# Kernel optimization log

Hardware: AMD Instinct MI355X
Metric: run time of the kernel (lower is better)

Reference implementation:

```python
import jax, jax.numpy as jnp
import numpy as np
from jax import lax

KS = 3
R = KS // 2
DILATIONS = (1, 3, 5)


def _fused_ddpm(x, kernels):
    """x: [N,C,H,W]; kernels: [N,3,C,KS*KS,H,W] -> [N,4C,H,W].
    Branch 0 is identity (x); branches 1..3 are per-pixel depthwise conv
    with dilations 1,3,5, zero padding, kernel taken at the output pixel."""
    N, C, H, W = x.shape
    outs = [x]
    for bi, d in enumerate(DILATIONS):
        pad = R * d
        xp = jnp.pad(x, ((0, 0), (0, 0), (pad, pad), (pad, pad)))
        acc = jnp.zeros_like(x)
        for ki in range(KS):
            for kj in range(KS):
                # shifted window: offset (ki-R)*d, (kj-R)*d relative to center
                patch = xp[:, :, ki * d:ki * d + H, kj * d:kj * d + W]
                acc = acc + patch * kernels[:, bi, :, ki * KS + kj]
        outs.append(acc)
    return jnp.concatenate(outs, axis=1)  # [N,4C,H,W]


def setup_inputs() -> dict:
    key = jax.random.key(0)
    k1, k2, k3, k4, k5, k6 = jax.random.split(key, 6)
    N, C, H, W = 4, 64, 128, 128
    x = jax.random.normal(k1, (N, C, H, W), dtype=jnp.float32)
    y = jax.random.normal(k2, (N, C, H, W), dtype=jnp.float32)
    # generator: Conv2d(C, 3*C*KS^2, 1) -> weight [3*C*9, C], bias [3*C*9]
    gen_w = jax.random.normal(k3, (3 * C * KS * KS, C), dtype=jnp.float32) * (1.0 / np.sqrt(C))
    gen_b = jax.random.normal(k4, (3 * C * KS * KS,), dtype=jnp.float32) * 0.01
    # fuse: Conv2d(4C, C, 3, 1, 1) -> weight [C, 4C, 3, 3], bias [C]
    fuse_w = jax.random.normal(k5, (C, 4 * C, 3, 3), dtype=jnp.float32) * (1.0 / np.sqrt(4 * C * 9))
    fuse_b = jax.random.normal(k6, (C,), dtype=jnp.float32) * 0.01
    return {"x": x, "y": y, "gen_w": gen_w, "gen_b": gen_b,
            "fuse_w": fuse_w, "fuse_b": fuse_b}


def reference(x, y, gen_w, gen_b, fuse_w, fuse_b):
    N, C, H, W = x.shape
    # 1x1 conv generator: per-pixel kernels
    k = jnp.einsum('oc,nchw->nohw', gen_w, y) + gen_b[None, :, None, None]
    kernels = k.reshape(N, 3, C, KS * KS, H, W)
    cat_out = _fused_ddpm(x, kernels)  # [N,4C,H,W]
    out = lax.conv_general_dilated(
        cat_out, fuse_w, window_strides=(1, 1), padding=((1, 1), (1, 1)),
        dimension_numbers=('NCHW', 'OIHW', 'NCHW'))
    return out + fuse_b[None, :, None, None]
```

## Files before the change

kernel.cpp:

```cpp
#include <hip/hip_runtime.h>


using f32x4 = __attribute__((ext_vector_type(4))) float;
using u32x4 = __attribute__((ext_vector_type(4))) unsigned;
using s16x8 = __attribute__((ext_vector_type(8))) short;

#define XP_PS 20160

#define OFF_WPK 0u
#define OFF_FW3 55296u
#define OFF_GBP 129024u
#define OFF_XP  131072u
#define OFF_CATP 4325376u

__device__ __forceinline__ unsigned short f2bf(float f) {
    unsigned u = __builtin_bit_cast(unsigned, f);
    u = (u + 0x7fffu + ((u >> 16) & 1u)) >> 16;
    return (unsigned short)u;
}
__device__ __forceinline__ float bflo(unsigned p) {
    return __builtin_bit_cast(float, p << 16);
}
__device__ __forceinline__ float bfhi(unsigned p) {
    return __builtin_bit_cast(float, p & 0xffff0000u);
}

__global__ void k_prep(const float* __restrict__ gen_w,
                       const float* __restrict__ gen_b,
                       const float* __restrict__ fuse_w,
                       const float* __restrict__ x,
                       float* __restrict__ ws) {
    int b = blockIdx.x;
    int t = threadIdx.x;
    if (b < 54) {
        int idx = b * 256 + t;
        if (idx >= 13824) return;
        unsigned short* wpk = (unsigned short*)(ws + OFF_WPK);
        int lane = idx & 63;
        int r = idx >> 6;
        int ks = r & 1; r >>= 1;
        int tile = r % 12, tap = r / 12;
        int comb = tile * 16 + (lane & 15);
        int cc0  = ks * 32 + (lane >> 4) * 8;
        const float* src = gen_w + (size_t)(comb * 9 + tap) * 64 + cc0;
        unsigned short v[8];
#pragma unroll
        for (int j = 0; j < 8; ++j) v[j] = f2bf(src[j]);
        *(s16x8*)(wpk + (size_t)idx * 8) = *(const s16x8*)v;
    } else if (b < 61) {
        int idx = (b - 54) * 256 + t;
        if (idx >= 1728) return;
        int row = idx & 15;
        int r = idx >> 4;
        int tile = r % 12, tap = r / 12;
        ws[OFF_GBP + idx] = gen_b[(tile * 16 + row) * 9 + tap];
    } else if (b < 133) {
        int idx = (b - 61) * 256 + t;
        if (idx >= 18432) return;
        unsigned short* fw3 = (unsigned short*)(ws + OFF_FW3);
        int lane = idx & 63;
        int f = idx >> 6;
        int rt = f & 3; f >>= 2;
        int ks = f & 1; f >>= 1;
        int chunk = f & 3;
        int g = f >> 2;
        int oc = rt * 16 + (lane & 15);
        int ic = chunk * 64 + ks * 32 + (lane >> 4) * 8;
        const float* src = fuse_w + (size_t)oc * 2304 + (size_t)ic * 9 + g;
        unsigned short v[8];
#pragma unroll
        for (int j = 0; j < 8; ++j) v[j] = f2bf(src[j * 9]);
        *(s16x8*)(fw3 + (size_t)idx * 8) = *(const s16x8*)v;
    } else {
        int idx = (b - 133) * 256 + t;
        unsigned* xp = (unsigned*)(ws + OFF_XP);
        int plane = idx / 5040;
        int rem   = idx % 5040;
        int row   = rem / 36;
        int c4    = rem % 36;
        u32x4 v = (u32x4){0u, 0u, 0u, 0u};
        if (row >= 5 && row < 133 && c4 >= 2 && c4 < 34) {
            const float* sx = x + (size_t)(2 * plane) * 16384 +
                              (row - 5) * 128 + (c4 * 4 - 8);
            f32x4 v0 = *(const f32x4*)sx;
            f32x4 v1 = *(const f32x4*)(sx + 16384);
#pragma unroll
            for (int j = 0; j < 4; ++j)
                v[j] = (unsigned)f2bf(v0[j]) | ((unsigned)f2bf(v1[j]) << 16);
        }
        *(u32x4*)(xp + (size_t)plane * XP_PS + row * 144 + c4 * 4) = v;
    }
}

__device__ __forceinline__ void decode_wu(int id, int& h, int& w0, int& n) {
    int wu = (id & 7) * 128 + (id >> 3);
    h = wu & 127;
    int sn = wu >> 7;
    w0 = (sn & 1) << 6;
    n = sn >> 1;
}

__global__ __launch_bounds__(256, 4) void k_gen_mfma(
    const unsigned* __restrict__ xp, const float* __restrict__ y,
    const unsigned short* __restrict__ wpk, const float* __restrict__ gbp,
    unsigned* __restrict__ catp)
{
    __shared__ __align__(16) unsigned Yt[2048];

    int h, w0, n;
    decode_wu(blockIdx.x, h, w0, n);
    const int t = threadIdx.x;
    const int lane = t & 63;
    const int wv = t >> 6;
    const int q = lane >> 4, col = lane & 15;

    {
        const float* yb = y + ((size_t)n * 64) * 16384 + h * 128 + w0 + lane;
#pragma unroll
        for (int p = 0; p < 8; ++p) {
            int cp = wv * 8 + p;
            float a = yb[(size_t)(2 * cp) * 16384];
            float b = yb[(size_t)(2 * cp + 1) * 16384];
            unsigned v = (unsigned)f2bf(a) | ((unsigned)f2bf(b) << 16);
            Yt[(unsigned)(lane * 32 + cp) ^ (((unsigned)(lane & 7)) << 2)] = v;
        }
    }
    __syncthreads();

    s16x8 bfr[4][2];
#pragma unroll
    for (int ctp = 0; ctp < 4; ++ctp)
#pragma unroll
        for (int ks = 0; ks < 2; ++ks) {
            int px = ctp * 16 + col;
            unsigned word = ((unsigned)(px * 32 + ks * 16 + q * 4)) ^
                            (((unsigned)(px & 7)) << 2);
            bfr[ctp][ks] = *(const s16x8*)(Yt + word);
        }

    const int tile0 = wv * 3;
    const unsigned* xn = xp + (size_t)n * 32 * XP_PS;

    float acc[3][4][4];
#pragma unroll
    for (int rt = 0; rt < 3; ++rt)
#pragma unroll
        for (int ctp = 0; ctp < 4; ++ctp)
#pragma unroll
            for (int r = 0; r < 4; ++r) acc[rt][ctp][r] = 0.f;

#pragma unroll 1
    for (int tap = 0; tap < 9; ++tap) {
        const int ti = tap / 3, tj = tap % 3;
        const unsigned short* wp = wpk + ((size_t)(tap * 12 + tile0) * 2 * 64 + lane) * 8;
#pragma unroll
        for (int rt = 0; rt < 3; ++rt) {
            const int tile = tile0 + rt;
            const int bi = tile >> 2;
            const int d  = 2 * bi + 1;
            const int hh = h + (ti - 1) * d;
            const int cb = (tile & 3) * 16 + q * 4;

            f32x4 cinit = *(const f32x4*)(gbp + (size_t)(tap * 12 + tile) * 16 + q * 4);
            s16x8 a0 = *(const s16x8*)(wp + (size_t)(rt * 2 + 0) * 512);
            s16x8 a1 = *(const s16x8*)(wp + (size_t)(rt * 2 + 1) * 512);
#pragma unroll
            for (int ctp = 0; ctp < 4; ++ctp) {
                f32x4 kf = __builtin_amdgcn_mfma_f32_16x16x32_bf16(a0, bfr[ctp][0], cinit, 0, 0, 0);
                kf = __builtin_amdgcn_mfma_f32_16x16x32_bf16(a1, bfr[ctp][1], kf, 0, 0, 0);
                const int ww = w0 + ctp * 16 + col + (tj - 1) * d;
                const unsigned* xr = xn + (size_t)(cb >> 1) * XP_PS +
                                     (hh + 5) * 144 + (ww + 8);
                unsigned p0 = xr[0];
                unsigned p1 = xr[XP_PS];
                acc[rt][ctp][0] = fmaf(kf[0], bflo(p0), acc[rt][ctp][0]);
                acc[rt][ctp][1] = fmaf(kf[1], bfhi(p0), acc[rt][ctp][1]);
                acc[rt][ctp][2] = fmaf(kf[2], bflo(p1), acc[rt][ctp][2]);
                acc[rt][ctp][3] = fmaf(kf[3], bfhi(p1), acc[rt][ctp][3]);
            }
        }
    }

    unsigned* cb0 = catp + (size_t)n * 96 * 16384 + h * 128;
#pragma unroll
    for (int rt = 0; rt < 3; ++rt) {
        const int combr = (tile0 + rt) * 16 + q * 4;
#pragma unroll
        for (int ctp = 0; ctp < 4; ++ctp) {
            const int px = w0 + ctp * 16 + col;
            unsigned v0 = (unsigned)f2bf(acc[rt][ctp][0]) |
                          ((unsigned)f2bf(acc[rt][ctp][1]) << 16);
            unsigned v1 = (unsigned)f2bf(acc[rt][ctp][2]) |
                          ((unsigned)f2bf(acc[rt][ctp][3]) << 16);
            cb0[(size_t)((combr >> 1) + 0) * 16384 + px] = v0;
            cb0[(size_t)((combr >> 1) + 1) * 16384 + px] = v1;
        }
    }
}

__global__ __launch_bounds__(256) void k_fuse_mfma(
    const unsigned* __restrict__ xp, const unsigned* __restrict__ catp,
    const unsigned short* __restrict__ fw3, const float* __restrict__ fuse_b,
    float* __restrict__ out)
{
    __shared__ __align__(16) unsigned Xt[4 * 32 * 68];

    const int id = blockIdx.x;
    const int xcd = id & 7;
    const int unit = id >> 3;
    const int h0 = unit << 1;
    const int n  = xcd >> 1;
    const int w0 = (xcd & 1) << 6;

    const int t = threadIdx.x;
    const int lane = t & 63;
    const int ctp = t >> 6;
    const int col = lane & 15, q = lane >> 4;

    int s_r[8], s_cp[8], s_li[8];
#pragma unroll
    for (int it = 0; it < 8; ++it) {
        int e = it * 256 + t;
        s_r[it]  = e >> 9;
        s_cp[it] = (e >> 4) & 31;
        s_li[it] = e & 15;
    }
    const int hr = t >> 6, hcp = (t >> 1) & 31, hside = t & 1;
    const int hpx = hside ? (w0 + 64) : (w0 - 1);
    const bool hok = ((unsigned)hpx < 128u);

    const int bcol = ctp * 16 + col;
    const int m_kw[3] = { (bcol == 0) ? 64 : bcol - 1,
                          bcol,
                          (bcol == 63) ? 65 : bcol + 1 };

    f32x4 acc[2][4];
#pragma unroll
    for (int row = 0; row < 2; ++row)
#pragma unroll
        for (int rt = 0; rt < 4; ++rt) acc[row][rt] = (f32x4){0.f, 0.f, 0.f, 0.f};

    const unsigned* csrc[4] = {
        nullptr,
        catp + (size_t)n * 96 * 16384,
        catp + ((size_t)n * 96 + 32) * 16384,
        catp + ((size_t)n * 96 + 64) * 16384 };

    u32x4 pf[8];
    unsigned pfh;
    {
        const unsigned* src0 = xp + (size_t)n * 32 * XP_PS;
#pragma unroll
        for (int it = 0; it < 8; ++it)
            pf[it] = *(const u32x4*)(src0 + (size_t)s_cp[it] * XP_PS +
                                     (h0 + 4 + s_r[it]) * 144 + 8 + w0 + s_li[it] * 4);
        pfh = src0[(size_t)hcp * XP_PS + (h0 + 4 + hr) * 144 + 8 + hpx];
    }

#pragma unroll 1
    for (int chunk = 0; chunk < 4; ++chunk) {
        s16x8 afc[4];
        {
            const unsigned short* ap =
                fw3 + ((size_t)(((chunk * 2 + 0) * 4) * 64 + lane)) * 8;
#pragma unroll
            for (int rt = 0; rt < 4; ++rt)
                afc[rt] = *(const s16x8*)(ap + (size_t)rt * 512);
        }

#pragma unroll
        for (int it = 0; it < 8; ++it)
            *(u32x4*)(Xt + (s_r[it] * 32 + s_cp[it]) * 68 + s_li[it] * 4) = pf[it];
        Xt[(hr * 32 + hcp) * 68 + 64 + hside] = pfh;

        if (chunk < 3) {
            const unsigned* src = csrc[chunk + 1];
#pragma unroll
            for (int it = 0; it < 8; ++it) {
                int hh = h0 - 1 + s_r[it];
                u32x4 v = (u32x4){0u, 0u, 0u, 0u};
                if ((unsigned)hh < 128u)
                    v = *(const u32x4*)(src + (size_t)s_cp[it] * 16384 + hh * 128 + w0 + s_li[it] * 4);
                pf[it] = v;
            }
            int hh = h0 - 1 + hr;
            unsigned v = 0u;
            if (hok && (unsigned)hh < 128u)
                v = src[(size_t)hcp * 16384 + hh * 128 + hpx];
            pfh = v;
        }
        __syncthreads();

#pragma unroll
        for (int i = 0; i < 18; ++i) {
            const int g = i >> 1, ks = i & 1;
            const int kh = g / 3, kw = g % 3;

            s16x8 afn[4];
            if (i < 17) {
                const int g2 = (i + 1) >> 1, ks2 = (i + 1) & 1;
                const unsigned short* ap = fw3 +
                    ((size_t)((((g2 * 4 + chunk) * 2 + ks2) * 4) * 64 + lane)) * 8;
#pragma unroll
                for (int rt = 0; rt < 4; ++rt)
                    afn[rt] = *(const s16x8*)(ap + (size_t)rt * 512);
            }

            const int cpb = ks * 16 + q * 4;
            const int mm = m_kw[kw];
            s16x8 bf[2];
#pragma unroll
            for (int row = 0; row < 2; ++row) {
                const unsigned* bp = Xt + ((row + kh) * 32 + cpb) * 68 + mm;
                unsigned bb[4] = {bp[0], bp[68], bp[136], bp[204]};
                bf[row] = *(const s16x8*)bb;
            }
#pragma unroll
            for (int rt = 0; rt < 4; ++rt)
#pragma unroll
                for (int row = 0; row < 2; ++row)
                    acc[row][rt] = __builtin_amdgcn_mfma_f32_16x16x32_bf16(
                        afc[rt], bf[row], acc[row][rt], 0, 0, 0);

            if (i < 17) {
#pragma unroll
                for (int rt = 0; rt < 4; ++rt) afc[rt] = afn[rt];
            }
        }
        __syncthreads();
    }

    const int px = w0 + ctp * 16 + col;
#pragma unroll
    for (int rt = 0; rt < 4; ++rt) {
        f32x4 fb = *(const f32x4*)(fuse_b + rt * 16 + q * 4);
#pragma unroll
        for (int row = 0; row < 2; ++row)
#pragma unroll
            for (int r = 0; r < 4; ++r) {
                int oc = rt * 16 + q * 4 + r;
                out[((size_t)n * 64 + oc) * 16384 + (h0 + row) * 128 + px] =
                    acc[row][rt][r] + fb[r];
            }
    }
}

extern "C" void kernel_launch(void* const* d_in, const int* in_sizes, int n_in,
                              void* d_out, int out_size, void* d_ws, size_t ws_size,
                              hipStream_t stream) {
    const float* x      = (const float*)d_in[0];
    const float* y      = (const float*)d_in[1];
    const float* gen_w  = (const float*)d_in[2];
    const float* gen_b  = (const float*)d_in[3];
    const float* fuse_w = (const float*)d_in[4];
    const float* fuse_b = (const float*)d_in[5];
    float* out = (float*)d_out;
    float* ws  = (float*)d_ws;

    unsigned* xp   = (unsigned*)(ws + OFF_XP);
    unsigned* catp = (unsigned*)(ws + OFF_CATP);

    k_prep<<<dim3(2653), dim3(256), 0, stream>>>(gen_w, gen_b, fuse_w, x, ws);
    k_gen_mfma<<<dim3(1024), dim3(256), 0, stream>>>(
        xp, y, (const unsigned short*)(ws + OFF_WPK), ws + OFF_GBP, catp);
    k_fuse_mfma<<<dim3(512), dim3(256), 0, stream>>>(
        xp, catp, (const unsigned short*)(ws + OFF_FW3), fuse_b, out);
}
```

Before: 83.67 us.

## Split fuse-conv K dimension across two waves per column tile with LDS reduction

The fuse kernel now launches 512 threads per block, and each pair of waves splits the channel half (ks) of every chunk's reduction. The 18-step MFMA loop becomes 9 steps per wave, and the partial sums are reduced through shared memory before the output store. The early barrier now sits before the next prefetch, so the loads overlap the MFMA work. This doubles wave-level parallelism per block to hide latency, at the cost of an extra LDS reduction, a barrier, and higher register pressure under the 512-thread launch bound.

```diff
diff --git a/kernel.cpp b/kernel.cpp
--- a/kernel.cpp
+++ b/kernel.cpp
@@ -198,7 +198,7 @@
     }
 }
 
-__global__ __launch_bounds__(256) void k_fuse_mfma(
+__global__ __launch_bounds__(512) void k_fuse_mfma(
     const unsigned* __restrict__ xp, const unsigned* __restrict__ catp,
     const unsigned short* __restrict__ fw3, const float* __restrict__ fuse_b,
     float* __restrict__ out)
@@ -214,20 +214,23 @@
 
     const int t = threadIdx.x;
     const int lane = t & 63;
-    const int ctp = t >> 6;
+    const int wv = t >> 6;
+    const int ctp = wv >> 1;
+    const int ks  = wv & 1;
     const int col = lane & 15, q = lane >> 4;
 
-    int s_r[8], s_cp[8], s_li[8];
-#pragma unroll
-    for (int it = 0; it < 8; ++it) {
-        int e = it * 256 + t;
+    int s_r[4], s_cp[4], s_li[4];
+#pragma unroll
+    for (int it = 0; it < 4; ++it) {
+        int e = it * 512 + t;
         s_r[it]  = e >> 9;
         s_cp[it] = (e >> 4) & 31;
         s_li[it] = e & 15;
     }
+    const bool hact = (t < 256);
     const int hr = t >> 6, hcp = (t >> 1) & 31, hside = t & 1;
     const int hpx = hside ? (w0 + 64) : (w0 - 1);
-    const bool hok = ((unsigned)hpx < 128u);
+    const bool hok = hact && ((unsigned)hpx < 128u);
 
     const int bcol = ctp * 16 + col;
     const int m_kw[3] = { (bcol == 0) ? 64 : bcol - 1,
@@ -246,15 +249,16 @@
         catp + ((size_t)n * 96 + 32) * 16384,
         catp + ((size_t)n * 96 + 64) * 16384 };
 
-    u32x4 pf[8];
-    unsigned pfh;
+    u32x4 pf[4];
+    unsigned pfh = 0u;
     {
         const unsigned* src0 = xp + (size_t)n * 32 * XP_PS;
 #pragma unroll
-        for (int it = 0; it < 8; ++it)
+        for (int it = 0; it < 4; ++it)
             pf[it] = *(const u32x4*)(src0 + (size_t)s_cp[it] * XP_PS +
                                      (h0 + 4 + s_r[it]) * 144 + 8 + w0 + s_li[it] * 4);
-        pfh = src0[(size_t)hcp * XP_PS + (h0 + 4 + hr) * 144 + 8 + hpx];
+        if (hact)
+            pfh = src0[(size_t)hcp * XP_PS + (h0 + 4 + hr) * 144 + 8 + hpx];
     }
 
 #pragma unroll 1
@@ -262,21 +266,24 @@
         s16x8 afc[4];
         {
             const unsigned short* ap =
-                fw3 + ((size_t)(((chunk * 2 + 0) * 4) * 64 + lane)) * 8;
+                fw3 + ((size_t)(((chunk * 2 + ks) * 4) * 64 + lane)) * 8;
 #pragma unroll
             for (int rt = 0; rt < 4; ++rt)
                 afc[rt] = *(const s16x8*)(ap + (size_t)rt * 512);
         }
 
 #pragma unroll
-        for (int it = 0; it < 8; ++it)
+        for (int it = 0; it < 4; ++it)
             *(u32x4*)(Xt + (s_r[it] * 32 + s_cp[it]) * 68 + s_li[it] * 4) = pf[it];
-        Xt[(hr * 32 + hcp) * 68 + 64 + hside] = pfh;
+        if (hact)
+            Xt[(hr * 32 + hcp) * 68 + 64 + hside] = pfh;
+
+        __syncthreads();
 
         if (chunk < 3) {
             const unsigned* src = csrc[chunk + 1];
 #pragma unroll
-            for (int it = 0; it < 8; ++it) {
+            for (int it = 0; it < 4; ++it) {
                 int hh = h0 - 1 + s_r[it];
                 u32x4 v = (u32x4){0u, 0u, 0u, 0u};
                 if ((unsigned)hh < 128u)
@@ -289,18 +296,15 @@
                 v = src[(size_t)hcp * 16384 + hh * 128 + hpx];
             pfh = v;
         }
-        __syncthreads();
-
-#pragma unroll
-        for (int i = 0; i < 18; ++i) {
-            const int g = i >> 1, ks = i & 1;
+
+#pragma unroll
+        for (int g = 0; g < 9; ++g) {
             const int kh = g / 3, kw = g % 3;
 
             s16x8 afn[4];
-            if (i < 17) {
-                const int g2 = (i + 1) >> 1, ks2 = (i + 1) & 1;
+            if (g < 8) {
                 const unsigned short* ap = fw3 +
-                    ((size_t)((((g2 * 4 + chunk) * 2 + ks2) * 4) * 64 + lane)) * 8;
+                    ((size_t)(((((g + 1) * 4 + chunk) * 2 + ks) * 4) * 64 + lane)) * 8;
 #pragma unroll
                 for (int rt = 0; rt < 4; ++rt)
                     afn[rt] = *(const s16x8*)(ap + (size_t)rt * 512);
@@ -322,7 +326,7 @@
                     acc[row][rt] = __builtin_amdgcn_mfma_f32_16x16x32_bf16(
                         afc[rt], bf[row], acc[row][rt], 0, 0, 0);
 
-            if (i < 17) {
+            if (g < 8) {
 #pragma unroll
                 for (int rt = 0; rt < 4; ++rt) afc[rt] = afn[rt];
             }
@@ -330,18 +334,33 @@
         __syncthreads();
     }
 
-    const int px = w0 + ctp * 16 + col;
-#pragma unroll
-    for (int rt = 0; rt < 4; ++rt) {
-        f32x4 fb = *(const f32x4*)(fuse_b + rt * 16 + q * 4);
+    float* red = (float*)Xt;
+    if (ks == 1) {
 #pragma unroll
         for (int row = 0; row < 2; ++row)
 #pragma unroll
-            for (int r = 0; r < 4; ++r) {
-                int oc = rt * 16 + q * 4 + r;
-                out[((size_t)n * 64 + oc) * 16384 + (h0 + row) * 128 + px] =
-                    acc[row][rt][r] + fb[r];
-            }
+            for (int rt = 0; rt < 4; ++rt)
+                *(f32x4*)(red + ((((ctp * 2 + row) * 4 + rt) * 64 + lane) << 2)) =
+                    acc[row][rt];
+    }
+    __syncthreads();
+    if (ks == 0) {
+        const int px = w0 + ctp * 16 + col;
+#pragma unroll
+        for (int rt = 0; rt < 4; ++rt) {
+            f32x4 fb = *(const f32x4*)(fuse_b + rt * 16 + q * 4);
+#pragma unroll
+            for (int row = 0; row < 2; ++row) {
+                f32x4 s = acc[row][rt] +
+                    *(const f32x4*)(red + ((((ctp * 2 + row) * 4 + rt) * 64 + lane) << 2));
+#pragma unroll
+                for (int r = 0; r < 4; ++r) {
+                    int oc = rt * 16 + q * 4 + r;
+                    out[((size_t)n * 64 + oc) * 16384 + (h0 + row) * 128 + px] =
+                        s[r] + fb[r];
+                }
+            }
+        }
     }
 }
 
@@ -363,6 +382,6 @@
     k_prep<<<dim3(2653), dim3(256), 0, stream>>>(gen_w, gen_b, fuse_w, x, ws);
     k_gen_mfma<<<dim3(1024), dim3(256), 0, stream>>>(
         xp, y, (const unsigned short*)(ws + OFF_WPK), ws + OFF_GBP, catp);
-    k_fuse_mfma<<<dim3(512), dim3(256), 0, stream>>>(
+    k_fuse_mfma<<<dim3(512), dim3(512), 0, stream>>>(
         xp, catp, (const unsigned short*)(ws + OFF_FW3), fuse_b, out);
 }
```

Result: slower. 90.64 us (+8.3%).
